# Performance work log

Measured on AMD Instinct MI355X. Metric: run time of the kernel, lower is better.

Reference implementation:

```python
import jax, jax.numpy as jnp
import numpy as np

CAPACITY = 8_388_608  # 2**23, power of two -> leftmost_leaf == capacity
N_UPDATES = 1_048_576  # 2**20


def setup_inputs() -> dict:
    key = jax.random.key(0)
    k1, k2, k3 = jax.random.split(key, 3)
    # Existing tree buffer; values[1] is root, values[CAPACITY:2*CAPACITY] are leaves.
    tree_values = jax.random.uniform(k1, (2 * CAPACITY,), dtype=jnp.float32)
    # Distinct leaf indices in [0, CAPACITY): torch scatter-assign with duplicate
    # indices is nondeterministic, so the meaningful case is distinct indices.
    indices = jax.random.permutation(k2, CAPACITY)[:N_UPDATES].astype(jnp.int32)
    values = jax.random.uniform(k3, (N_UPDATES,), dtype=jnp.float32)
    return {"tree_values": tree_values, "indices": indices, "values": values}


def reference(tree_values, indices, values):
    """SegmentTree.__setitem__ with op=add: set leaves, propagate sums to root.

    Returns the updated (2*capacity,) tree buffer.
    """
    capacity = tree_values.shape[0] // 2  # static python int
    depth = int(capacity).bit_length() - 1  # log2(capacity) levels to the root
    # _index_to_leaf: with power-of-two capacity, leaf = idx + capacity (no wrap).
    leaf = indices.astype(jnp.int32) + capacity
    tree = tree_values.at[leaf].set(values)
    idx = leaf
    # Original does torch.unique(idx//2) per level purely as an optimization;
    # duplicate parents recompute the identical value, so plain scatter-set of
    # op(left_child, right_child) is the same math and jit-friendly.
    for _ in range(depth):
        idx = idx // 2
        parent = tree[2 * idx] + tree[2 * idx + 1]
        tree = tree.at[idx].set(parent)
    return tree
```

## Files before the change

### kernel.cpp

```cpp
#include <hip/hip_runtime.h>


typedef unsigned int uint;
typedef unsigned char uchar;
typedef unsigned long long ull;

#define NB_COARSE 256
#define CCAP 4608
#define FCAP 512
#define NPB 4096

__device__ __forceinline__ ull pc64(ull c) {
    ull x = (c | (c >> 1)) & 0x5555555555555555ull;
    x = (x | (x >> 1))  & 0x3333333333333333ull;
    x = (x | (x >> 2))  & 0x0F0F0F0F0F0F0F0Full;
    x = (x | (x >> 4))  & 0x00FF00FF00FF00FFull;
    x = (x | (x >> 8))  & 0x0000FFFF0000FFFFull;
    x = (x | (x >> 16)) & 0x00000000FFFFFFFFull;
    return x;
}

__global__ void clear_kernel(uint* __restrict__ gcursor) {
    gcursor[threadIdx.x] = threadIdx.x * CCAP;
}

__global__ __launch_bounds__(256)
void coarse_bin_kernel(const int* __restrict__ idx,
                       const float* __restrict__ val,
                       uint* __restrict__ gcursor,
                       uint2* __restrict__ coarse) {
    __shared__ uint hist[NB_COARSE], rbase[NB_COARSE], cur[NB_COARSE];
    const int tid = threadIdx.x;
    hist[tid] = 0u;
    __syncthreads();

    const int i0 = blockIdx.x * NPB;
    uint j[16]; float v[16];
    #pragma unroll
    for (int e = 0; e < 16; ++e) {
        int i = i0 + e * 256 + tid;
        j[e] = (uint)idx[i];
        v[e] = val[i];
        atomicAdd(&hist[j[e] >> 15], 1u);
    }
    __syncthreads();
    rbase[tid] = hist[tid] ? atomicAdd(&gcursor[tid], hist[tid]) : 0u;
    cur[tid] = 0u;
    __syncthreads();
    #pragma unroll
    for (int e = 0; e < 16; ++e) {
        uint cb = j[e] >> 15;
        uint pos = rbase[cb] + atomicAdd(&cur[cb], 1u);
        if (pos < (cb + 1u) * CCAP)
            coarse[pos] = make_uint2(j[e], __float_as_uint(v[e]));
    }
}

__global__ __launch_bounds__(256)
void fine_bin_kernel(const uint* __restrict__ gcursor,
                     const uint2* __restrict__ coarse,
                     uint* __restrict__ fcnt,
                     uint2* __restrict__ fbins) {
    __shared__ uint fcur[16];
    const int b = blockIdx.x, tid = threadIdx.x;
    if (tid < 16) fcur[tid] = 0u;
    __syncthreads();
    uint nb = gcursor[b] - (uint)b * CCAP;
    if (nb > CCAP) nb = CCAP;
    const uint2* my = coarse + (size_t)b * CCAP;
    for (uint k = tid; k < nb; k += 256u) {
        uint2 e = my[k];
        uint fb = (e.x >> 11) & 15u;
        uint r = atomicAdd(&fcur[fb], 1u);
        if (r < FCAP)
            fbins[(((size_t)b * 16u + fb) << 9) + r] = e;
    }
    __syncthreads();
    if (tid < 16) {
        uint c = fcur[tid];
        fcnt[b * 16 + tid] = c > FCAP ? FCAP : c;
    }
}

__global__ __launch_bounds__(256)
void merge_kernel(const float* __restrict__ tree,
                  const uint* __restrict__ fcnt,
                  const uint2* __restrict__ fbins,
                  uchar* __restrict__ l11flag,
                  float* __restrict__ out, int C) {
    __shared__ float slv[2048];
    __shared__ uchar sfl[2048];
    __shared__ float swv[4];
    __shared__ uint  swd[4];

    const int b   = blockIdx.x;
    const int tid = threadIdx.x;
    const int w    = tid >> 6;
    const int lane = tid & 63;

    ((uint2*)sfl)[tid] = make_uint2(0u, 0u);
    __syncthreads();
    uint c = fcnt[b];
    const uint2* mybin = fbins + ((size_t)b << 9);
    for (uint k = tid; k < c; k += 256u) {
        uint2 e = mybin[k];
        uint off = e.x & 2047u;
        slv[off] = __uint_as_float(e.y);
        sfl[off] = 1;
    }
    __syncthreads();

    const int leaf0  = tid * 8;
    const int gleaf0 = b * 2048 + leaf0;

    uint2 fw = *(const uint2*)&sfl[leaf0];
    float4 la = *(const float4*)&slv[leaf0];
    float4 lb = *(const float4*)&slv[leaf0 + 4];
    float4 ta = *(const float4*)(tree + C + gleaf0);
    float4 tb = *(const float4*)(tree + C + gleaf0 + 4);

    float l0 = (fw.x & 0x000000FFu) ? la.x : ta.x;
    float l1 = (fw.x & 0x0000FF00u) ? la.y : ta.y;
    float l2 = (fw.x & 0x00FF0000u) ? la.z : ta.z;
    float l3 = (fw.x & 0xFF000000u) ? la.w : ta.w;
    float l4 = (fw.y & 0x000000FFu) ? lb.x : tb.x;
    float l5 = (fw.y & 0x0000FF00u) ? lb.y : tb.y;
    float l6 = (fw.y & 0x00FF0000u) ? lb.z : tb.z;
    float l7 = (fw.y & 0xFF000000u) ? lb.w : tb.w;

    *(float4*)(out + C + gleaf0)     = make_float4(l0, l1, l2, l3);
    *(float4*)(out + C + gleaf0 + 4) = make_float4(l4, l5, l6, l7);

    uint d10 = (fw.x & 0x0000FFFFu) != 0u;
    uint d11 = (fw.x & 0xFFFF0000u) != 0u;
    uint d12 = (fw.y & 0x0000FFFFu) != 0u;
    uint d13 = (fw.y & 0xFFFF0000u) != 0u;
    float4 t1 = *(const float4*)(tree + (C >> 1) + (gleaf0 >> 1));
    float4 v1;
    v1.x = d10 ? l0 + l1 : t1.x;
    v1.y = d11 ? l2 + l3 : t1.y;
    v1.z = d12 ? l4 + l5 : t1.z;
    v1.w = d13 ? l6 + l7 : t1.w;
    *(float4*)(out + (C >> 1) + (gleaf0 >> 1)) = v1;

    float2 t2 = *(const float2*)(tree + (C >> 2) + (gleaf0 >> 2));
    uint d20 = d10 | d11, d21 = d12 | d13;
    float2 v2;
    v2.x = d20 ? v1.x + v1.y : t2.x;
    v2.y = d21 ? v1.z + v1.w : t2.y;
    *(float2*)(out + (C >> 2) + (gleaf0 >> 2)) = v2;

    float t3 = tree[(C >> 3) + (gleaf0 >> 3)];
    uint d3 = d20 | d21;
    float v = d3 ? v2.x + v2.y : t3;
    out[(C >> 3) + (gleaf0 >> 3)] = v;

    ull m = __ballot(d3 != 0u);
    #pragma unroll
    for (int lvl = 4; lvl <= 9; ++lvl) {
        float a  = __shfl(v, 2 * lane, 64);
        float bb = __shfl(v, 2 * lane + 1, 64);
        m = pc64(m);
        int n = 64 >> (lvl - 3);
        if (lane < n) {
            int node = (C >> lvl) + ((b * 2048 + w * 512) >> lvl) + lane;
            uint d = (uint)(m >> lane) & 1u;
            v = d ? a + bb : tree[node];
            out[node] = v;
        }
    }

    if (lane == 0) { swv[w] = v; swd[w] = (uint)(m & 1ull); }
    __syncthreads();
    if (tid == 0) {
        uint da0 = swd[0] | swd[1], da1 = swd[2] | swd[3];
        int n10 = (C >> 10) + 2 * b;
        float v100 = da0 ? swv[0] + swv[1] : tree[n10];
        float v101 = da1 ? swv[2] + swv[3] : tree[n10 + 1];
        out[n10]     = v100;
        out[n10 + 1] = v101;
        uint d11f = da0 | da1;
        int n11 = (C >> 11) + b;
        out[n11] = d11f ? v100 + v101 : tree[n11];
        l11flag[b] = (uchar)d11f;
    }
}

__global__ __launch_bounds__(1024)
void tail_kernel(const float* __restrict__ tree,
                 const uchar* __restrict__ l11flag,
                 float* __restrict__ out) {
    __shared__ float s16[16];
    __shared__ uint  sd16[16];
    const int t = threadIdx.x, w = t >> 6, lane = t & 63;

    float4 ch = *(const float4*)(out + 4096 + 4 * t);
    uint fl = ((const uint*)l11flag)[t];
    uint d0 = (fl & 0x0000FFFFu) != 0u;
    uint d1 = (fl & 0xFFFF0000u) != 0u;
    float2 t12 = *(const float2*)(tree + 2048 + 2 * t);
    float v0 = d0 ? ch.x + ch.y : t12.x;
    float v1 = d1 ? ch.z + ch.w : t12.y;
    *(float2*)(out + 2048 + 2 * t) = make_float2(v0, v1);
    uint d = d0 | d1;
    float v = d ? v0 + v1 : tree[1024 + t];
    out[1024 + t] = v;

    ull m = __ballot(d != 0u);
    #pragma unroll
    for (int M = 512; M >= 16; M >>= 1) {
        float a  = __shfl(v, 2 * lane, 64);
        float bb = __shfl(v, 2 * lane + 1, 64);
        m = pc64(m);
        int nw = M >> 4;
        if (lane < nw) {
            int node = M + nw * w + lane;
            uint dd = (uint)(m >> lane) & 1u;
            v = dd ? a + bb : tree[node];
            out[node] = v;
        }
    }
    if (lane == 0) { s16[w] = v; sd16[w] = (uint)(m & 1ull); }
    __syncthreads();

    if (w == 0) {
        float vv = lane < 16 ? s16[lane] : 0.f;
        uint dd  = lane < 16 ? sd16[lane] : 0u;
        ull mm = __ballot(dd != 0u);
        #pragma unroll
        for (int M = 8; M >= 1; M >>= 1) {
            float a  = __shfl(vv, 2 * lane, 64);
            float bb = __shfl(vv, 2 * lane + 1, 64);
            mm = pc64(mm);
            if (lane < M) {
                uint d2 = (uint)(mm >> lane) & 1u;
                vv = d2 ? a + bb : tree[M + lane];
                out[M + lane] = vv;
            }
        }
        if (lane == 0) out[0] = tree[0];
    }
}

extern "C" void kernel_launch(void* const* d_in, const int* in_sizes, int n_in,
                              void* d_out, int out_size, void* d_ws, size_t ws_size,
                              hipStream_t stream) {
    const float* tree    = (const float*)d_in[0];
    const int*   indices = (const int*)d_in[1];
    const float* values  = (const float*)d_in[2];
    float* out = (float*)d_out;

    const int two_cap = in_sizes[0];
    const int C       = two_cap >> 1;

    uchar* ws = (uchar*)d_ws;
    uint*  gcursor = (uint*)ws;
    uint*  fcnt    = (uint*)(ws + 1024);
    uchar* l11     = ws + 17408;
    uint2* coarse  = (uint2*)(ws + 32768);
    uint2* fbins   = (uint2*)(ws + 32768 + (size_t)NB_COARSE * CCAP * 8);

    clear_kernel<<<1, NB_COARSE, 0, stream>>>(gcursor);
    coarse_bin_kernel<<<NB_COARSE, 256, 0, stream>>>(indices, values,
                                                     gcursor, coarse);
    fine_bin_kernel<<<NB_COARSE, 256, 0, stream>>>(gcursor, coarse,
                                                   fcnt, fbins);
    merge_kernel<<<C / 2048, 256, 0, stream>>>(tree, fcnt, fbins, l11, out, C);
    tail_kernel<<<1, 1024, 0, stream>>>(tree, l11, out);
}
```

Measured before the change: 159.4 us.

## Replace two-pass coarse/fine binning with single-pass direct binning into 4096 bins

Merges the coarse binning and fine binning kernels into one kernel. Each 1024-thread block histograms its 4096 updates over 4096 fine bins in shared memory, reserves ranges with global atomics, and scatters straight into the per-merge-block bins. This removes one kernel launch and the write and re-read of the intermediate coarse buffer. In exchange it issues many more global atomics (up to 4096 per block) and does more scattered small writes, and the merge kernel now clamps counts that can exceed capacity.

```diff
diff --git a/kernel.cpp b/kernel.cpp
--- a/kernel.cpp
+++ b/kernel.cpp
@@ -5,10 +5,8 @@
 typedef unsigned char uchar;
 typedef unsigned long long ull;
 
-#define NB_COARSE 256
-#define CCAP 4608
-#define FCAP 512
-#define NPB 4096
+#define NBINS 4096
+#define FCAP  512
 
 __device__ __forceinline__ ull pc64(ull c) {
     ull x = (c | (c >> 1)) & 0x5555555555555555ull;
@@ -20,65 +18,49 @@
     return x;
 }
 
-__global__ void clear_kernel(uint* __restrict__ gcursor) {
-    gcursor[threadIdx.x] = threadIdx.x * CCAP;
-}
-
-__global__ __launch_bounds__(256)
-void coarse_bin_kernel(const int* __restrict__ idx,
-                       const float* __restrict__ val,
-                       uint* __restrict__ gcursor,
-                       uint2* __restrict__ coarse) {
-    __shared__ uint hist[NB_COARSE], rbase[NB_COARSE], cur[NB_COARSE];
+__global__ void clear_kernel(uint* __restrict__ fcnt) {
+    fcnt[blockIdx.x * 256 + threadIdx.x] = 0u;
+}
+
+__global__ __launch_bounds__(1024)
+void bin_kernel(const int* __restrict__ idx,
+                const float* __restrict__ val,
+                uint* __restrict__ fcnt,
+                uint2* __restrict__ fbins) {
+    __shared__ uint hist[NBINS];
+    __shared__ uint rbase[NBINS];
     const int tid = threadIdx.x;
-    hist[tid] = 0u;
-    __syncthreads();
-
-    const int i0 = blockIdx.x * NPB;
-    uint j[16]; float v[16];
-    #pragma unroll
-    for (int e = 0; e < 16; ++e) {
-        int i = i0 + e * 256 + tid;
-        j[e] = (uint)idx[i];
-        v[e] = val[i];
-        atomicAdd(&hist[j[e] >> 15], 1u);
-    }
-    __syncthreads();
-    rbase[tid] = hist[tid] ? atomicAdd(&gcursor[tid], hist[tid]) : 0u;
-    cur[tid] = 0u;
-    __syncthreads();
-    #pragma unroll
-    for (int e = 0; e < 16; ++e) {
-        uint cb = j[e] >> 15;
-        uint pos = rbase[cb] + atomicAdd(&cur[cb], 1u);
-        if (pos < (cb + 1u) * CCAP)
-            coarse[pos] = make_uint2(j[e], __float_as_uint(v[e]));
-    }
-}
-
-__global__ __launch_bounds__(256)
-void fine_bin_kernel(const uint* __restrict__ gcursor,
-                     const uint2* __restrict__ coarse,
-                     uint* __restrict__ fcnt,
-                     uint2* __restrict__ fbins) {
-    __shared__ uint fcur[16];
-    const int b = blockIdx.x, tid = threadIdx.x;
-    if (tid < 16) fcur[tid] = 0u;
-    __syncthreads();
-    uint nb = gcursor[b] - (uint)b * CCAP;
-    if (nb > CCAP) nb = CCAP;
-    const uint2* my = coarse + (size_t)b * CCAP;
-    for (uint k = tid; k < nb; k += 256u) {
-        uint2 e = my[k];
-        uint fb = (e.x >> 11) & 15u;
-        uint r = atomicAdd(&fcur[fb], 1u);
+
+    #pragma unroll
+    for (int e = 0; e < 4; ++e) hist[e * 1024 + tid] = 0u;
+    __syncthreads();
+
+    const int base4 = blockIdx.x * 1024 + tid;
+    int4   j4 = ((const int4*)idx)[base4];
+    float4 v4 = ((const float4*)val)[base4];
+    uint  j[4] = { (uint)j4.x, (uint)j4.y, (uint)j4.z, (uint)j4.w };
+    float v[4] = { v4.x, v4.y, v4.z, v4.w };
+
+    #pragma unroll
+    for (int e = 0; e < 4; ++e) atomicAdd(&hist[j[e] >> 11], 1u);
+    __syncthreads();
+
+    #pragma unroll
+    for (int e = 0; e < 4; ++e) {
+        int bin = e * 1024 + tid;
+        uint h = hist[bin];
+        rbase[bin] = h ? atomicAdd(&fcnt[bin], h) : 0u;
+        hist[bin] = 0u;
+    }
+    __syncthreads();
+
+    #pragma unroll
+    for (int e = 0; e < 4; ++e) {
+        uint bin = j[e] >> 11;
+        uint r = rbase[bin] + atomicAdd(&hist[bin], 1u);
         if (r < FCAP)
-            fbins[(((size_t)b * 16u + fb) << 9) + r] = e;
-    }
-    __syncthreads();
-    if (tid < 16) {
-        uint c = fcur[tid];
-        fcnt[b * 16 + tid] = c > FCAP ? FCAP : c;
+            fbins[((size_t)bin << 9) + r] =
+                make_uint2(j[e] & 2047u, __float_as_uint(v[e]));
     }
 }
 
@@ -101,6 +83,7 @@
     ((uint2*)sfl)[tid] = make_uint2(0u, 0u);
     __syncthreads();
     uint c = fcnt[b];
+    if (c > FCAP) c = FCAP;
     const uint2* mybin = fbins + ((size_t)b << 9);
     for (uint k = tid; k < c; k += 256u) {
         uint2 e = mybin[k];
@@ -254,17 +237,12 @@
     const int C       = two_cap >> 1;
 
     uchar* ws = (uchar*)d_ws;
-    uint*  gcursor = (uint*)ws;
-    uint*  fcnt    = (uint*)(ws + 1024);
-    uchar* l11     = ws + 17408;
-    uint2* coarse  = (uint2*)(ws + 32768);
-    uint2* fbins   = (uint2*)(ws + 32768 + (size_t)NB_COARSE * CCAP * 8);
-
-    clear_kernel<<<1, NB_COARSE, 0, stream>>>(gcursor);
-    coarse_bin_kernel<<<NB_COARSE, 256, 0, stream>>>(indices, values,
-                                                     gcursor, coarse);
-    fine_bin_kernel<<<NB_COARSE, 256, 0, stream>>>(gcursor, coarse,
-                                                   fcnt, fbins);
+    uint*  fcnt  = (uint*)ws;
+    uchar* l11   = ws + 16384;
+    uint2* fbins = (uint2*)(ws + 32768);
+
+    clear_kernel<<<16, 256, 0, stream>>>(fcnt);
+    bin_kernel<<<256, 1024, 0, stream>>>(indices, values, fcnt, fbins);
     merge_kernel<<<C / 2048, 256, 0, stream>>>(tree, fcnt, fbins, l11, out, C);
     tail_kernel<<<1, 1024, 0, stream>>>(tree, l11, out);
 }
```

Measured after the change: 151.0 us. 1.06x faster.
